# Kernel optimization log

Measured on AMD Instinct MI355X. Metric: run time of the kernel, lower is better.

Reference implementation:

```python
import jax, jax.numpy as jnp
import numpy as np

FEATURE_DIM = 16
NUM_HEADS = 16
HEAD_DIM = 64
R2 = float(np.sqrt(2.0))
RD = float(np.sqrt(FEATURE_DIM))        # sqrt(d) = 4
RRD = float(np.sqrt(RD))                # d^(1/4) = 2
RMS_EPS = 1e-5


def taylor_exp(x):
    # x: [b, h, l, d] -> [b, h, l, 1 + d + d*d]
    x2 = (x[..., :, None] * x[..., None, :]).reshape(*x.shape[:-1], FEATURE_DIM * FEATURE_DIM) / R2
    ones = jnp.ones_like(x[..., :1])
    return jnp.concatenate([ones, x / RRD, x2 / RD], axis=-1)


def setup_inputs() -> dict:
    key = jax.random.key(0)
    ks = jax.random.split(key, 5)
    b, l, d_model = 4, 2048, 1024
    inp = {
        'hidden_states': jax.random.normal(ks[0], (b, l, d_model), dtype=jnp.float32),
        'Wq': jax.random.normal(ks[1], (FEATURE_DIM * NUM_HEADS, d_model), dtype=jnp.float32) * 0.02,
        'Wk': jax.random.normal(ks[2], (FEATURE_DIM * NUM_HEADS, d_model), dtype=jnp.float32) * 0.02,
        'Wv': jax.random.normal(ks[3], (NUM_HEADS * HEAD_DIM, d_model), dtype=jnp.float32) * 0.02,
        'Wo': jax.random.normal(ks[4], (d_model, NUM_HEADS * HEAD_DIM), dtype=jnp.float32) * 0.02,
        'g_weight': jnp.ones((HEAD_DIM,), dtype=jnp.float32),
    }
    return inp


def reference(hidden_states, Wq, Wk, Wv, Wo, g_weight):
    b, l, _ = hidden_states.shape
    # projections (Linear, no bias): x @ W.T
    q = (hidden_states @ Wq.T).reshape(b, l, NUM_HEADS, FEATURE_DIM).transpose(0, 2, 1, 3)
    k = (hidden_states @ Wk.T).reshape(b, l, NUM_HEADS, FEATURE_DIM).transpose(0, 2, 1, 3)
    v = (hidden_states @ Wv.T).reshape(b, l, NUM_HEADS, HEAD_DIM).transpose(0, 2, 1, 3)

    qf = taylor_exp(q)  # [b, h, l, 273]
    kf = taylor_exp(k)  # [b, h, l, 273]

    A_qk = jnp.einsum('bhnd,bhmd->bhnm', qf, kf)
    A_qk = jnp.tril(A_qk)
    y = jnp.einsum('bhnm,bhme->bhne', A_qk, v)  # [b, h, l, head_dim]

    kv_state = jnp.einsum('bhnd,bhnf->bhfd', kf, v)[:, :, None]  # [b, h, 1, head_dim, 273]

    # RMSNorm over head_dim
    rms = jax.lax.rsqrt(jnp.mean(y * y, axis=-1, keepdims=True) + RMS_EPS)
    y = y * rms * g_weight

    y = y.transpose(0, 2, 1, 3).reshape(b, l, NUM_HEADS * HEAD_DIM)
    out = y @ Wo.T
    return out, kv_state
```

## Files before the change

kernel.cpp:

```cpp
#include <hip/hip_runtime.h>


typedef unsigned short u16;
typedef unsigned int u32;
typedef __attribute__((ext_vector_type(4))) float f32x4;
typedef __attribute__((ext_vector_type(16))) float f32x16;
typedef __attribute__((ext_vector_type(8))) short s16x8;

struct MaskT { static constexpr bool value = true;  };
struct MaskF { static constexpr bool value = false; };

__device__ __forceinline__ float bf2f(u16 u) {
    union { unsigned int i; float f; } x; x.i = ((unsigned int)u) << 16; return x.f;
}
__device__ __forceinline__ u16 f2bf(float f) {
    union { float f; unsigned int u; } x; x.f = f;
    unsigned int r = x.u + 0x7FFFu + ((x.u >> 16) & 1u);
    return (u16)(r >> 16);
}

typedef const __attribute__((address_space(1))) u32* gas1_t;
typedef __attribute__((address_space(3))) u32* las3_t;
__device__ __forceinline__ void gld16(const u16* g, u16* l) {
    __builtin_amdgcn_global_load_lds((gas1_t)(const void*)g, (las3_t)(void*)l, 16, 0, 0);
}

__global__ void detect_kernel(const unsigned int* __restrict__ H, int* __restrict__ flag)
{
    const int lane = threadIdx.x;
    int cnt = 0;
#pragma unroll
    for (int i = 0; i < 16; ++i) {
        const unsigned int wrd = H[lane * 16 + i];
        const int e = (int)((wrd >> 7) & 0xFFu);
        if (e >= 85 && e <= 170) ++cnt;
    }
    cnt += __shfl_xor(cnt, 1);  cnt += __shfl_xor(cnt, 2);
    cnt += __shfl_xor(cnt, 4);  cnt += __shfl_xor(cnt, 8);
    cnt += __shfl_xor(cnt, 16); cnt += __shfl_xor(cnt, 32);
    if (lane == 0) *flag = (cnt < 700) ? 1 : 0;
}

__global__ __launch_bounds__(256)
void cvt_all_kernel(const void* __restrict__ H,  const void* __restrict__ Wq,
                    const void* __restrict__ Wk, const void* __restrict__ Wv,
                    const void* __restrict__ Wo, const void* __restrict__ gw,
                    u16* __restrict__ Hb,  u16* __restrict__ Wqb,
                    u16* __restrict__ Wkb, u16* __restrict__ Wvb,
                    u16* __restrict__ Wob, u16* __restrict__ gwb,
                    const int* __restrict__ flag)
{
    const int f32in = *flag;
    const int NQ = 11010112 / 4;
    for (int qi = blockIdx.x * 256 + threadIdx.x; qi < NQ; qi += gridDim.x * 256) {
        const int i = qi * 4;
        const void* src; u16* dst; int off;
        if      (i <  8388608) { src = H;  dst = Hb;  off = i; }
        else if (i <  8650752) { src = Wq; dst = Wqb; off = i - 8388608; }
        else if (i <  8912896) { src = Wk; dst = Wkb; off = i - 8650752; }
        else if (i <  9961472) { src = Wv; dst = Wvb; off = i - 8912896; }
        else if (i < 11010048) { src = Wo; dst = Wob; off = i - 9961472; }
        else                   { src = gw; dst = gwb; off = i - 11010048; }
        ushort4 o;
        if (f32in) {
            const float4 v = *((const float4*)src + (off >> 2));
            o.x = f2bf(v.x); o.y = f2bf(v.y); o.z = f2bf(v.z); o.w = f2bf(v.w);
        } else {
            o = *((const ushort4*)src + (off >> 2));
        }
        *(ushort4*)(dst + off) = o;
    }
}

template<int MODE>
__global__ __launch_bounds__(256)
void gemm_nt(const u16* __restrict__ A,
             const u16* __restrict__ Bq, const u16* __restrict__ Bk,
             const u16* __restrict__ Bv,
             u16* __restrict__ Oq, u16* __restrict__ Ok,
             u16* __restrict__ Ovt, float* __restrict__ Of)
{
    __shared__ __attribute__((aligned(16))) u16 As[8192];
    __shared__ __attribute__((aligned(16))) u16 Bs[8192];
    const int t = threadIdx.x;
    const int lane = t & 63, w = t >> 6;
    const int c = lane & 15, qd = lane >> 4;
    const int wm = (w >> 1) * 64, wn = (w & 1) * 64;
    const int nwgx = gridDim.x;
    const int pid = blockIdx.y * nwgx + blockIdx.x;
    const int lid = (pid & 7) * ((nwgx * 64) >> 3) + (pid >> 3);
    const int rm = (lid / nwgx) * 128;
    const int cb = (lid % nwgx) * 128;

    const u16* Bsrc; int wrow0;
    if (MODE == 0) {
        if (cb < 256)      { Bsrc = Bq; wrow0 = cb; }
        else if (cb < 512) { Bsrc = Bk; wrow0 = cb - 256; }
        else               { Bsrc = Bv; wrow0 = cb - 512; }
    } else { Bsrc = Bq; wrow0 = cb; }

    f32x4 acc[4][4];
#pragma unroll
    for (int i = 0; i < 4; ++i)
#pragma unroll
        for (int j = 0; j < 4; ++j) acc[i][j] = (f32x4){0.f, 0.f, 0.f, 0.f};

    const int r0 = w * 8 + (lane >> 3);
    const int s0 = (lane & 7) ^ (lane >> 3);
    const u16* Ag = A    + (size_t)(rm    + r0) * 1024 + s0 * 8;
    const u16* Bg = Bsrc + (size_t)(wrow0 + r0) * 1024 + s0 * 8;
    u16* AsW = As + w * 512;
    u16* BsW = Bs + w * 512;

    for (int kt = 0; kt < 16; ++kt) {
        const int k0 = kt * 64;
        __syncthreads();
#pragma unroll
        for (int i = 0; i < 4; ++i) {
            gld16(Ag + (size_t)(i * 32) * 1024 + k0, AsW + i * 2048);
            gld16(Bg + (size_t)(i * 32) * 1024 + k0, BsW + i * 2048);
        }
        __syncthreads();
        s16x8 af[2][4], bfr[2][4];
#pragma unroll
        for (int kk = 0; kk < 2; ++kk) {
#pragma unroll
            for (int mt = 0; mt < 4; ++mt) {
                const int row = wm + mt * 16 + c;
                af[kk][mt] = *(const s16x8*)&As[row * 64 + (((kk * 4 + qd) ^ (row & 7)) * 8)];
            }
#pragma unroll
            for (int nt = 0; nt < 4; ++nt) {
                const int row = wn + nt * 16 + c;
                bfr[kk][nt] = *(const s16x8*)&Bs[row * 64 + (((kk * 4 + qd) ^ (row & 7)) * 8)];
            }
        }
#pragma unroll
        for (int kk = 0; kk < 2; ++kk)
#pragma unroll
            for (int mt = 0; mt < 4; ++mt)
#pragma unroll
                for (int nt = 0; nt < 4; ++nt)
                    acc[mt][nt] = __builtin_amdgcn_mfma_f32_16x16x32_bf16(af[kk][mt], bfr[kk][nt], acc[mt][nt], 0, 0, 0);
    }

#pragma unroll
    for (int mt = 0; mt < 4; ++mt) {
#pragma unroll
        for (int nt = 0; nt < 4; ++nt) {
            const int gc = cb + wn + nt * 16 + c;
            const int row0 = rm + wm + mt * 16 + qd * 4;
            if (MODE == 1) {
#pragma unroll
                for (int r = 0; r < 4; ++r)
                    Of[(size_t)(row0 + r) * 1024 + gc] = acc[mt][nt][r];
            } else if (gc < 512) {
#pragma unroll
                for (int r = 0; r < 4; ++r) {
                    const int row = row0 + r;
                    const int b_ = row >> 11, l_ = row & 2047;
                    const int cc = gc & 255;
                    const int h = cc >> 4, idx = cc & 15;
                    u16* dst = (gc < 256) ? Oq : Ok;
                    dst[(size_t)((b_ * 16 + h) * 2048 + l_) * 16 + idx] = f2bf(acc[mt][nt][r]);
                }
            } else {
                const int cc = gc - 512;
                const int h = cc >> 6, idx = cc & 63;
                const int b_ = row0 >> 11, l0 = row0 & 2047;
                ushort4 pk;
                pk.x = f2bf(acc[mt][nt][0]);
                pk.y = f2bf(acc[mt][nt][1]);
                pk.z = f2bf(acc[mt][nt][2]);
                pk.w = f2bf(acc[mt][nt][3]);
                *(ushort4*)(Ovt + ((size_t)((b_ * 16 + h) * 64 + idx)) * 2048 + l0) = pk;
            }
        }
    }
}

__global__ __launch_bounds__(512, 4)
void attn_kernel(const u16* __restrict__ Qg, const u16* __restrict__ Kg,
                 const u16* __restrict__ Vt, const u16* __restrict__ gwb,
                 u16* __restrict__ Yn)
{
    __shared__ __attribute__((aligned(16))) u16 Vs[2][8192];
    const int t = threadIdx.x, lane = t & 63, w = t >> 6;
    const int la = lane & 31, h = lane >> 5;
    const int pid = blockIdx.y * 8 + blockIdx.x;
    const int x = pid & 7;
    const int yy = pid >> 3;
    const int bh = x * 8 + (yy >> 3);
    const int jj = yy & 3;
    const int pass = (yy >> 2) & 1;
    const int qb = pass ? jj : (7 - jj);
    const int b_ = bh >> 4, hh = bh & 15;
    const u16* Qh = Qg + (size_t)bh * (2048 * 16);
    const u16* Kh = Kg + (size_t)bh * (2048 * 16);
    const u16* Vh = Vt + (size_t)bh * (64 * 2048);
    const float gl0 = bf2f(gwb[la]);
    const float gl1 = bf2f(gwb[32 + la]);
    const f32x16 z16 = {0.f,0.f,0.f,0.f,0.f,0.f,0.f,0.f,
                        0.f,0.f,0.f,0.f,0.f,0.f,0.f,0.f};
    const int vbase0 = (la << 8) | (h << 4);
    const int vsw = (la & 7) << 4;

    auto stageV = [&](int n0s, int bufsel) {
#pragma unroll
        for (int i = 0; i < 2; ++i) {
            const int slot = i * 512 + t;
            const int fl = slot >> 4;
            const int seg = (slot & 15) ^ (fl & 7);
            gld16(Vh + (size_t)fl * 2048 + n0s + seg * 8,
                  (u16*)Vs[bufsel] + (size_t)(i * 512 + (w << 6)) * 8);
        }
    };

    const int q0 = qb * 256 + w * 32;
    const int kf = 2 * qb + (w >> 2);
    const int wp = w & 3;
    const int nck = 2 * qb + 2;

    const s16x8 bq = *(const s16x8*)(Qh + (size_t)(q0 + la) * 16 + h * 8);
    f32x16 yt0 = z16, yt1 = z16;
    s16x8 ka[4];
    const char* vsc = (const char*)Vs[0];

    auto loadK = [&](s16x8* kk, int kcL) {
#pragma unroll
        for (int kt = 0; kt < 4; ++kt)
            kk[kt] = *(const s16x8*)(Kh + (size_t)(kcL * 128 + kt * 32 + la) * 16 + h * 8);
    };

    auto tile = [&](int kt, auto MASKED) {
        constexpr bool masked = decltype(MASKED)::value;
        f32x16 sv = __builtin_amdgcn_mfma_f32_32x32x16_bf16(ka[kt], bq, z16, 0, 0, 0);
        float p[16];
#pragma unroll
        for (int r = 0; r < 16; ++r) {
            const float s = sv[r];
            float pv = fmaf(s, fmaf(s, 0.03125f, 0.25f), 1.0f);
            if (masked) {
                const int keyloc = (r & 3) + 8 * (r >> 2) + 4 * h;
                if (keyloc > la) pv = 0.f;
            }
            p[r] = pv;
        }
#pragma unroll
        for (int ks = 0; ks < 2; ++ks) {
            u32 X0, X1, Y0, Y1;
            asm("v_cvt_pk_bf16_f32 %0, %1, %2" : "=v"(X0) : "v"(p[8*ks+0]), "v"(p[8*ks+1]));
            asm("v_cvt_pk_bf16_f32 %0, %1, %2" : "=v"(X1) : "v"(p[8*ks+2]), "v"(p[8*ks+3]));
            asm("v_cvt_pk_bf16_f32 %0, %1, %2" : "=v"(Y0) : "v"(p[8*ks+4]), "v"(p[8*ks+5]));
            asm("v_cvt_pk_bf16_f32 %0, %1, %2" : "=v"(Y1) : "v"(p[8*ks+6]), "v"(p[8*ks+7]));
            asm("v_permlane32_swap_b32 %0, %1" : "+v"(X0), "+v"(Y0));
            asm("v_permlane32_swap_b32 %0, %1" : "+v"(X1), "+v"(Y1));
            union { uint4 u; s16x8 v; } afu;
            afu.u = (uint4){X0, X1, Y0, Y1};
            const int offb = (kt << 6) | (ks << 5);
            const s16x8 vb0 = *(const s16x8*)(vsc + (((vbase0 + offb)) ^ vsw));
            const s16x8 vb1 = *(const s16x8*)(vsc + (((vbase0 + 8192 + offb)) ^ vsw));
            yt0 = __builtin_amdgcn_mfma_f32_32x32x16_bf16(afu.v, vb0, yt0, 0, 0, 0);
            yt1 = __builtin_amdgcn_mfma_f32_32x32x16_bf16(afu.v, vb1, yt1, 0, 0, 0);
        }
    };

    stageV(0, 0);
    loadK(ka, 0);
    __syncthreads();

    for (int kc = 0; kc < nck; ++kc) {
        const int cur = kc & 1;
        vsc = (const char*)Vs[cur];
        if (kc + 1 < nck) stageV((kc + 1) * 128, cur ^ 1);
        s16x8 kn[4] = {ka[0], ka[1], ka[2], ka[3]};
        if (kc < kf) loadK(kn, kc + 1);

        if (kc < kf) {
            tile(0, MaskF{}); tile(1, MaskF{});
            tile(2, MaskF{}); tile(3, MaskF{});
        } else if (kc == kf) {
            if (wp == 0)      { tile(0, MaskT{}); }
            else if (wp == 1) { tile(0, MaskF{}); tile(1, MaskT{}); }
            else if (wp == 2) { tile(0, MaskF{}); tile(1, MaskF{}); tile(2, MaskT{}); }
            else              { tile(0, MaskF{}); tile(1, MaskF{}); tile(2, MaskF{}); tile(3, MaskT{}); }
        }
        __syncthreads();
#pragma unroll
        for (int kt = 0; kt < 4; ++kt) ka[kt] = kn[kt];
    }

#pragma unroll
    for (int r = 0; r < 16; ++r) {
        float ss = yt0[r] * yt0[r] + yt1[r] * yt1[r];
        ss += __shfl_xor(ss, 1);  ss += __shfl_xor(ss, 2);
        ss += __shfl_xor(ss, 4);  ss += __shfl_xor(ss, 8);
        ss += __shfl_xor(ss, 16);
        const float rmsv = rsqrtf(ss * (1.0f / 64.0f) + 1e-5f);
        const int row = q0 + (r & 3) + 8 * (r >> 2) + 4 * h;
        u16* dst = Yn + ((size_t)(b_ * 2048 + row)) * 1024 + hh * 64;
        dst[la]      = f2bf(yt0[r] * rmsv * gl0);
        dst[32 + la] = f2bf(yt1[r] * rmsv * gl1);
    }
}

__global__ __launch_bounds__(256)
void kv_mfma_kernel(const u16* __restrict__ Kg, const u16* __restrict__ Vt,
                    float* __restrict__ kvpart)
{
    __shared__ __attribute__((aligned(16))) float kS[64][20];
    __shared__ __attribute__((aligned(16))) float kT[64][20];
    __shared__ __attribute__((aligned(16))) u16 KFs[288][72];
    __shared__ __attribute__((aligned(16))) u16 Vs[64][72];
    const int t = threadIdx.x, lane = t & 63, w = t >> 6;
    const int c = lane & 15, qd = lane >> 4;
    const int ns = blockIdx.x, bh = blockIdx.y;
    const u16* Kh  = Kg + (size_t)bh * 2048 * 16;
    const u16* Vth = Vt + (size_t)bh * 64 * 2048;

    int i2a, j2a, i2b = 18, j2b = 18;
    {
        const int dd = t;
        if (dd == 0)      { i2a = 16; j2a = 17; }
        else if (dd < 17) { i2a = dd - 1; j2a = 16; }
        else              { i2a = (dd - 17) >> 4; j2a = (dd - 17) & 15; }
        if (t < 32) {
            const int d2 = 256 + t;
            if (d2 < 273) { i2b = (d2 - 17) >> 4; j2b = (d2 - 17) & 15; }
        }
    }

    f32x4 acc[4][5];
#pragma unroll
    for (int mt = 0; mt < 4; ++mt)
#pragma unroll
        for (int j = 0; j < 5; ++j) acc[mt][j] = (f32x4){0.f, 0.f, 0.f, 0.f};

    for (int ch = 0; ch < 8; ++ch) {
        const int n0 = ns * 512 + ch * 64;
        __syncthreads();
        if (t < 128) {
            const int row = t >> 1, half = t & 1;
            uint4 kv = *(const uint4*)(Kh + (size_t)(n0 + row) * 16 + half * 8);
            const u16* ke = (const u16*)&kv;
#pragma unroll
            for (int e = 0; e < 8; ++e) {
                const float f = bf2f(ke[e]);
                kS[row][half * 8 + e] = f;
                kT[row][half * 8 + e] = f * 0.17677669529663687f;
            }
        } else if (t < 192) {
            const int row = t - 128;
            kS[row][16] = 1.f;  kS[row][17] = 1.f;  kS[row][18] = 0.f;
            kT[row][16] = 0.5f; kT[row][17] = 1.f;  kT[row][18] = 0.f;
        }
#pragma unroll
        for (int i = 0; i < 2; ++i) {
            const int lin = i * 256 + t;
            const int f = lin >> 3, seg = lin & 7;
            *(uint4*)&Vs[f][seg * 8] =
                *(const uint4*)(Vth + (size_t)f * 2048 + n0 + seg * 8);
        }
        __syncthreads();
        {
            unsigned int* dst = (unsigned int*)&KFs[t][0];
#pragma unroll 8
            for (int i = 0; i < 32; ++i) {
                const float v0 = kS[2 * i][i2a]     * kT[2 * i][j2a];
                const float v1 = kS[2 * i + 1][i2a] * kT[2 * i + 1][j2a];
                dst[i] = (unsigned int)f2bf(v0) | ((unsigned int)f2bf(v1) << 16);
            }
            if (t < 32) {
                unsigned int* dst2 = (unsigned int*)&KFs[256 + t][0];
#pragma unroll 8
                for (int i = 0; i < 32; ++i) {
                    const float v0 = kS[2 * i][i2b]     * kT[2 * i][j2b];
                    const float v1 = kS[2 * i + 1][i2b] * kT[2 * i + 1][j2b];
                    dst2[i] = (unsigned int)f2bf(v0) | ((unsigned int)f2bf(v1) << 16);
                }
            }
        }
        __syncthreads();
#pragma unroll
        for (int kt = 0; kt < 2; ++kt) {
            s16x8 va[4];
#pragma unroll
            for (int mt = 0; mt < 4; ++mt)
                va[mt] = *(const s16x8*)&Vs[mt * 16 + c][kt * 32 + qd * 8];
#pragma unroll
            for (int j = 0; j < 5; ++j) {
                const int dt = w + 4 * j;
                if (dt < 18) {
                    s16x8 vb = *(const s16x8*)&KFs[dt * 16 + c][kt * 32 + qd * 8];
#pragma unroll
                    for (int mt = 0; mt < 4; ++mt)
                        acc[mt][j] = __builtin_amdgcn_mfma_f32_16x16x32_bf16(va[mt], vb, acc[mt][j], 0, 0, 0);
                }
            }
        }
    }

    float* base = kvpart + ((size_t)(ns * 64 + bh) * 64) * 273;
#pragma unroll
    for (int j = 0; j < 5; ++j) {
        const int dt = w + 4 * j;
        if (dt >= 18) continue;
        const int dd = dt * 16 + c;
        if (dd >= 273) continue;
#pragma unroll
        for (int mt = 0; mt < 4; ++mt)
#pragma unroll
            for (int r = 0; r < 4; ++r) {
                const int f = mt * 16 + qd * 4 + r;
                base[f * 273 + dd] = acc[mt][j][r];
            }
    }
}

__global__ __launch_bounds__(256)
void kv_fin_kernel(const float* __restrict__ kvpart, float* __restrict__ o)
{
    const int i = blockIdx.x * 256 + threadIdx.x;
    const int S = 64 * 64 * 273;
    if (i < S)
        o[i] = kvpart[i] + kvpart[i + S] + kvpart[i + 2 * S] + kvpart[i + 3 * S];
}

extern "C" void kernel_launch(void* const* d_in, const int* in_sizes, int n_in,
                              void* d_out, int out_size, void* d_ws, size_t ws_size,
                              hipStream_t stream)
{
    const void* H  = d_in[0];
    const void* Wq = d_in[1];
    const void* Wk = d_in[2];
    const void* Wv = d_in[3];
    const void* Wo = d_in[4];
    const void* gw = d_in[5];
    float* outf = (float*)d_out;

    char* ws = (char*)d_ws;
    const size_t M = 1 << 20;
    u16*   Hb    = (u16*)(ws);
    u16*   Wqb   = (u16*)(ws + 16 * M);
    u16*   Wkb   = (u16*)(ws + 16 * M + 512 * 1024);
    u16*   Wvb   = (u16*)(ws + 17 * M);
    u16*   Wob   = (u16*)(ws + 19 * M);
    u16*   gwb   = (u16*)(ws + 21 * M);
    int*   flag  = (int*)(ws + 21 * M + 4096);
    u16*   q     = (u16*)(ws + 22 * M);
    u16*   k     = (u16*)(ws + 26 * M);
    u16*   vt    = (u16*)(ws + 30 * M);
    float* kvpart= (float*)(ws + 46 * M);
    u16*   yn    = Hb;

    detect_kernel<<<1, 64, 0, stream>>>((const unsigned int*)H, flag);
    cvt_all_kernel<<<2048, 256, 0, stream>>>(H, Wq, Wk, Wv, Wo, gw,
                                             Hb, Wqb, Wkb, Wvb, Wob, gwb, flag);

    gemm_nt<0><<<dim3(12, 64), 256, 0, stream>>>(Hb, Wqb, Wkb, Wvb, q, k, vt, nullptr);
    attn_kernel<<<dim3(8, 64), 512, 0, stream>>>(q, k, vt, gwb, yn);
    kv_mfma_kernel<<<dim3(4, 64), 256, 0, stream>>>(k, vt, kvpart);
    kv_fin_kernel<<<4368, 256, 0, stream>>>(kvpart, outf + (size_t)8388608);
    gemm_nt<1><<<dim3(8, 64), 256, 0, stream>>>(yn, Wob, nullptr, nullptr,
                                                nullptr, nullptr, nullptr, outf);
}
```

Before: 241.1 us.

## Fuse dtype detect and kv reduction into neighbors, merge attention passes per block

Folds the input-dtype detection into every block of the conversion kernel and the kv partial-sum reduction into the tail of the output-projection GEMM, removing two kernel launches. The attention kernel now runs both causal query-block passes (a long and a short one) inside a single workgroup, which halves the grid and balances work per block. It also relaxes launch bounds from 4 to 2 waves per SIMD and widens the LDS swizzle from 8 to 16 segments. The cost is less parallelism in attention and extra tail work in every GEMM block.

Measured after the change: 228.1 us. 5.4% less time.

```diff
diff --git a/kernel.cpp b/kernel.cpp
--- a/kernel.cpp
+++ b/kernel.cpp
@@ -23,22 +23,6 @@
 typedef __attribute__((address_space(3))) u32* las3_t;
 __device__ __forceinline__ void gld16(const u16* g, u16* l) {
     __builtin_amdgcn_global_load_lds((gas1_t)(const void*)g, (las3_t)(void*)l, 16, 0, 0);
-}
-
-__global__ void detect_kernel(const unsigned int* __restrict__ H, int* __restrict__ flag)
-{
-    const int lane = threadIdx.x;
-    int cnt = 0;
-#pragma unroll
-    for (int i = 0; i < 16; ++i) {
-        const unsigned int wrd = H[lane * 16 + i];
-        const int e = (int)((wrd >> 7) & 0xFFu);
-        if (e >= 85 && e <= 170) ++cnt;
-    }
-    cnt += __shfl_xor(cnt, 1);  cnt += __shfl_xor(cnt, 2);
-    cnt += __shfl_xor(cnt, 4);  cnt += __shfl_xor(cnt, 8);
-    cnt += __shfl_xor(cnt, 16); cnt += __shfl_xor(cnt, 32);
-    if (lane == 0) *flag = (cnt < 700) ? 1 : 0;
 }
 
 __global__ __launch_bounds__(256)
@@ -47,12 +31,29 @@
                     const void* __restrict__ Wo, const void* __restrict__ gw,
                     u16* __restrict__ Hb,  u16* __restrict__ Wqb,
                     u16* __restrict__ Wkb, u16* __restrict__ Wvb,
-                    u16* __restrict__ Wob, u16* __restrict__ gwb,
-                    const int* __restrict__ flag)
+                    u16* __restrict__ Wob, u16* __restrict__ gwb)
 {
-    const int f32in = *flag;
+    __shared__ int sflag;
+    const int t = threadIdx.x;
+    if (t < 64) {
+        const unsigned int* Hw = (const unsigned int*)H;
+        int cnt = 0;
+#pragma unroll
+        for (int i = 0; i < 16; ++i) {
+            const unsigned int wrd = Hw[t * 16 + i];
+            const int e = (int)((wrd >> 7) & 0xFFu);
+            if (e >= 85 && e <= 170) ++cnt;
+        }
+        cnt += __shfl_xor(cnt, 1);  cnt += __shfl_xor(cnt, 2);
+        cnt += __shfl_xor(cnt, 4);  cnt += __shfl_xor(cnt, 8);
+        cnt += __shfl_xor(cnt, 16); cnt += __shfl_xor(cnt, 32);
+        if (t == 0) sflag = (cnt < 700) ? 1 : 0;
+    }
+    __syncthreads();
+    const int f32in = sflag;
+
     const int NQ = 11010112 / 4;
-    for (int qi = blockIdx.x * 256 + threadIdx.x; qi < NQ; qi += gridDim.x * 256) {
+    for (int qi = blockIdx.x * 256 + t; qi < NQ; qi += gridDim.x * 256) {
         const int i = qi * 4;
         const void* src; u16* dst; int off;
         if      (i <  8388608) { src = H;  dst = Hb;  off = i; }
@@ -78,7 +79,8 @@
              const u16* __restrict__ Bq, const u16* __restrict__ Bk,
              const u16* __restrict__ Bv,
              u16* __restrict__ Oq, u16* __restrict__ Ok,
-             u16* __restrict__ Ovt, float* __restrict__ Of)
+             u16* __restrict__ Ovt, float* __restrict__ Of,
+             const float* __restrict__ Kvp, float* __restrict__ Kvo)
 {
     __shared__ __attribute__((aligned(16))) u16 As[8192];
     __shared__ __attribute__((aligned(16))) u16 Bs[8192];
@@ -177,9 +179,24 @@
             }
         }
     }
-}
-
-__global__ __launch_bounds__(512, 4)
+
+    if (MODE == 1) {
+        const int S = 64 * 64 * 273;
+        const int NQ4 = S / 4;
+        const int NT = gridDim.x * gridDim.y * 256;
+        for (int q = pid * 256 + t; q < NQ4; q += NT) {
+            float4 a = ((const float4*)Kvp)[q];
+            const float4 b = ((const float4*)(Kvp + S))[q];
+            const float4 c2 = ((const float4*)(Kvp + 2 * S))[q];
+            const float4 d = ((const float4*)(Kvp + 3 * S))[q];
+            a.x += b.x + c2.x + d.x;  a.y += b.y + c2.y + d.y;
+            a.z += b.z + c2.z + d.z;  a.w += b.w + c2.w + d.w;
+            ((float4*)Kvo)[q] = a;
+        }
+    }
+}
+
+__global__ __launch_bounds__(512, 2)
 void attn_kernel(const u16* __restrict__ Qg, const u16* __restrict__ Kg,
                  const u16* __restrict__ Vt, const u16* __restrict__ gwb,
                  u16* __restrict__ Yn)
@@ -187,13 +204,10 @@
     __shared__ __attribute__((aligned(16))) u16 Vs[2][8192];
     const int t = threadIdx.x, lane = t & 63, w = t >> 6;
     const int la = lane & 31, h = lane >> 5;
-    const int pid = blockIdx.y * 8 + blockIdx.x;
-    const int x = pid & 7;
-    const int yy = pid >> 3;
-    const int bh = x * 8 + (yy >> 3);
-    const int jj = yy & 3;
-    const int pass = (yy >> 2) & 1;
-    const int qb = pass ? jj : (7 - jj);
+    const int pid = blockIdx.y * 4 + blockIdx.x;
+    const int lid = (pid & 7) * 32 + (pid >> 3);
+    const int bh = lid >> 2;
+    const int jj = lid & 3;
     const int b_ = bh >> 4, hh = bh & 15;
     const u16* Qh = Qg + (size_t)bh * (2048 * 16);
     const u16* Kh = Kg + (size_t)bh * (2048 * 16);
@@ -203,104 +217,107 @@
     const f32x16 z16 = {0.f,0.f,0.f,0.f,0.f,0.f,0.f,0.f,
                         0.f,0.f,0.f,0.f,0.f,0.f,0.f,0.f};
     const int vbase0 = (la << 8) | (h << 4);
-    const int vsw = (la & 7) << 4;
+    const int vsw = (la & 15) << 4;
 
     auto stageV = [&](int n0s, int bufsel) {
 #pragma unroll
         for (int i = 0; i < 2; ++i) {
             const int slot = i * 512 + t;
             const int fl = slot >> 4;
-            const int seg = (slot & 15) ^ (fl & 7);
+            const int seg = (slot & 15) ^ (fl & 15);
             gld16(Vh + (size_t)fl * 2048 + n0s + seg * 8,
                   (u16*)Vs[bufsel] + (size_t)(i * 512 + (w << 6)) * 8);
         }
     };
 
-    const int q0 = qb * 256 + w * 32;
-    const int kf = 2 * qb + (w >> 2);
-    const int wp = w & 3;
-    const int nck = 2 * qb + 2;
-
-    const s16x8 bq = *(const s16x8*)(Qh + (size_t)(q0 + la) * 16 + h * 8);
-    f32x16 yt0 = z16, yt1 = z16;
-    s16x8 ka[4];
-    const char* vsc = (const char*)Vs[0];
-
-    auto loadK = [&](s16x8* kk, int kcL) {
-#pragma unroll
-        for (int kt = 0; kt < 4; ++kt)
-            kk[kt] = *(const s16x8*)(Kh + (size_t)(kcL * 128 + kt * 32 + la) * 16 + h * 8);
-    };
-
-    auto tile = [&](int kt, auto MASKED) {
-        constexpr bool masked = decltype(MASKED)::value;
-        f32x16 sv = __builtin_amdgcn_mfma_f32_32x32x16_bf16(ka[kt], bq, z16, 0, 0, 0);
-        float p[16];
+    for (int pass = 0; pass < 2; ++pass) {
+        const int qb = pass ? jj : (7 - jj);
+        const int q0 = qb * 256 + w * 32;
+        const int kf = 2 * qb + (w >> 2);
+        const int wp = w & 3;
+        const int nck = 2 * qb + 2;
+
+        const s16x8 bq = *(const s16x8*)(Qh + (size_t)(q0 + la) * 16 + h * 8);
+        f32x16 yt0 = z16, yt1 = z16;
+        s16x8 ka[4];
+        const char* vsc = (const char*)Vs[0];
+
+        auto loadK = [&](s16x8* kk, int kcL) {
+#pragma unroll
+            for (int kt = 0; kt < 4; ++kt)
+                kk[kt] = *(const s16x8*)(Kh + (size_t)(kcL * 128 + kt * 32 + la) * 16 + h * 8);
+        };
+
+        auto tile = [&](int kt, auto MASKED) {
+            constexpr bool masked = decltype(MASKED)::value;
+            f32x16 sv = __builtin_amdgcn_mfma_f32_32x32x16_bf16(ka[kt], bq, z16, 0, 0, 0);
+            float p[16];
+#pragma unroll
+            for (int r = 0; r < 16; ++r) {
+                const float s = sv[r];
+                float pv = fmaf(s, fmaf(s, 0.03125f, 0.25f), 1.0f);
+                if (masked) {
+                    const int keyloc = (r & 3) + 8 * (r >> 2) + 4 * h;
+                    if (keyloc > la) pv = 0.f;
+                }
+                p[r] = pv;
+            }
+#pragma unroll
+            for (int ks = 0; ks < 2; ++ks) {
+                u32 X0, X1, Y0, Y1;
+                asm("v_cvt_pk_bf16_f32 %0, %1, %2" : "=v"(X0) : "v"(p[8*ks+0]), "v"(p[8*ks+1]));
+                asm("v_cvt_pk_bf16_f32 %0, %1, %2" : "=v"(X1) : "v"(p[8*ks+2]), "v"(p[8*ks+3]));
+                asm("v_cvt_pk_bf16_f32 %0, %1, %2" : "=v"(Y0) : "v"(p[8*ks+4]), "v"(p[8*ks+5]));
+                asm("v_cvt_pk_bf16_f32 %0, %1, %2" : "=v"(Y1) : "v"(p[8*ks+6]), "v"(p[8*ks+7]));
+                asm("v_permlane32_swap_b32 %0, %1" : "+v"(X0), "+v"(Y0));
+                asm("v_permlane32_swap_b32 %0, %1" : "+v"(X1), "+v"(Y1));
+                union { uint4 u; s16x8 v; } afu;
+                afu.u = (uint4){X0, X1, Y0, Y1};
+                const int offb = (kt << 6) | (ks << 5);
+                const s16x8 vb0 = *(const s16x8*)(vsc + (((vbase0 + offb)) ^ vsw));
+                const s16x8 vb1 = *(const s16x8*)(vsc + (((vbase0 + 8192 + offb)) ^ vsw));
+                yt0 = __builtin_amdgcn_mfma_f32_32x32x16_bf16(afu.v, vb0, yt0, 0, 0, 0);
+                yt1 = __builtin_amdgcn_mfma_f32_32x32x16_bf16(afu.v, vb1, yt1, 0, 0, 0);
+            }
+        };
+
+        stageV(0, 0);
+        loadK(ka, 0);
+        __syncthreads();
+
+        for (int kc = 0; kc < nck; ++kc) {
+            const int cur = kc & 1;
+            vsc = (const char*)Vs[cur];
+            if (kc + 1 < nck) stageV((kc + 1) * 128, cur ^ 1);
+            s16x8 kn[4] = {ka[0], ka[1], ka[2], ka[3]};
+            if (kc < kf) loadK(kn, kc + 1);
+
+            if (kc < kf) {
+                tile(0, MaskF{}); tile(1, MaskF{});
+                tile(2, MaskF{}); tile(3, MaskF{});
+            } else if (kc == kf) {
+                if (wp == 0)      { tile(0, MaskT{}); }
+                else if (wp == 1) { tile(0, MaskF{}); tile(1, MaskT{}); }
+                else if (wp == 2) { tile(0, MaskF{}); tile(1, MaskF{}); tile(2, MaskT{}); }
+                else              { tile(0, MaskF{}); tile(1, MaskF{}); tile(2, MaskF{}); tile(3, MaskT{}); }
+            }
+            __syncthreads();
+#pragma unroll
+            for (int kt = 0; kt < 4; ++kt) ka[kt] = kn[kt];
+        }
+
 #pragma unroll
         for (int r = 0; r < 16; ++r) {
-            const float s = sv[r];
-            float pv = fmaf(s, fmaf(s, 0.03125f, 0.25f), 1.0f);
-            if (masked) {
-                const int keyloc = (r & 3) + 8 * (r >> 2) + 4 * h;
-                if (keyloc > la) pv = 0.f;
-            }
-            p[r] = pv;
-        }
-#pragma unroll
-        for (int ks = 0; ks < 2; ++ks) {
-            u32 X0, X1, Y0, Y1;
-            asm("v_cvt_pk_bf16_f32 %0, %1, %2" : "=v"(X0) : "v"(p[8*ks+0]), "v"(p[8*ks+1]));
-            asm("v_cvt_pk_bf16_f32 %0, %1, %2" : "=v"(X1) : "v"(p[8*ks+2]), "v"(p[8*ks+3]));
-            asm("v_cvt_pk_bf16_f32 %0, %1, %2" : "=v"(Y0) : "v"(p[8*ks+4]), "v"(p[8*ks+5]));
-            asm("v_cvt_pk_bf16_f32 %0, %1, %2" : "=v"(Y1) : "v"(p[8*ks+6]), "v"(p[8*ks+7]));
-            asm("v_permlane32_swap_b32 %0, %1" : "+v"(X0), "+v"(Y0));
-            asm("v_permlane32_swap_b32 %0, %1" : "+v"(X1), "+v"(Y1));
-            union { uint4 u; s16x8 v; } afu;
-            afu.u = (uint4){X0, X1, Y0, Y1};
-            const int offb = (kt << 6) | (ks << 5);
-            const s16x8 vb0 = *(const s16x8*)(vsc + (((vbase0 + offb)) ^ vsw));
-            const s16x8 vb1 = *(const s16x8*)(vsc + (((vbase0 + 8192 + offb)) ^ vsw));
-            yt0 = __builtin_amdgcn_mfma_f32_32x32x16_bf16(afu.v, vb0, yt0, 0, 0, 0);
-            yt1 = __builtin_amdgcn_mfma_f32_32x32x16_bf16(afu.v, vb1, yt1, 0, 0, 0);
-        }
-    };
-
-    stageV(0, 0);
-    loadK(ka, 0);
-    __syncthreads();
-
-    for (int kc = 0; kc < nck; ++kc) {
-        const int cur = kc & 1;
-        vsc = (const char*)Vs[cur];
-        if (kc + 1 < nck) stageV((kc + 1) * 128, cur ^ 1);
-        s16x8 kn[4] = {ka[0], ka[1], ka[2], ka[3]};
-        if (kc < kf) loadK(kn, kc + 1);
-
-        if (kc < kf) {
-            tile(0, MaskF{}); tile(1, MaskF{});
-            tile(2, MaskF{}); tile(3, MaskF{});
-        } else if (kc == kf) {
-            if (wp == 0)      { tile(0, MaskT{}); }
-            else if (wp == 1) { tile(0, MaskF{}); tile(1, MaskT{}); }
-            else if (wp == 2) { tile(0, MaskF{}); tile(1, MaskF{}); tile(2, MaskT{}); }
-            else              { tile(0, MaskF{}); tile(1, MaskF{}); tile(2, MaskF{}); tile(3, MaskT{}); }
-        }
-        __syncthreads();
-#pragma unroll
-        for (int kt = 0; kt < 4; ++kt) ka[kt] = kn[kt];
-    }
-
-#pragma unroll
-    for (int r = 0; r < 16; ++r) {
-        float ss = yt0[r] * yt0[r] + yt1[r] * yt1[r];
-        ss += __shfl_xor(ss, 1);  ss += __shfl_xor(ss, 2);
-        ss += __shfl_xor(ss, 4);  ss += __shfl_xor(ss, 8);
-        ss += __shfl_xor(ss, 16);
-        const float rmsv = rsqrtf(ss * (1.0f / 64.0f) + 1e-5f);
-        const int row = q0 + (r & 3) + 8 * (r >> 2) + 4 * h;
-        u16* dst = Yn + ((size_t)(b_ * 2048 + row)) * 1024 + hh * 64;
-        dst[la]      = f2bf(yt0[r] * rmsv * gl0);
-        dst[32 + la] = f2bf(yt1[r] * rmsv * gl1);
+            float ss = yt0[r] * yt0[r] + yt1[r] * yt1[r];
+            ss += __shfl_xor(ss, 1);  ss += __shfl_xor(ss, 2);
+            ss += __shfl_xor(ss, 4);  ss += __shfl_xor(ss, 8);
+            ss += __shfl_xor(ss, 16);
+            const float rmsv = rsqrtf(ss * (1.0f / 64.0f) + 1e-5f);
+            const int row = q0 + (r & 3) + 8 * (r >> 2) + 4 * h;
+            u16* dst = Yn + ((size_t)(b_ * 2048 + row)) * 1024 + hh * 64;
+            dst[la]      = f2bf(yt0[r] * rmsv * gl0);
+            dst[32 + la] = f2bf(yt1[r] * rmsv * gl1);
+        }
     }
 }
 
@@ -417,15 +434,6 @@
     }
 }
 
-__global__ __launch_bounds__(256)
-void kv_fin_kernel(const float* __restrict__ kvpart, float* __restrict__ o)
-{
-    const int i = blockIdx.x * 256 + threadIdx.x;
-    const int S = 64 * 64 * 273;
-    if (i < S)
-        o[i] = kvpart[i] + kvpart[i + S] + kvpart[i + 2 * S] + kvpart[i + 3 * S];
-}
-
 extern "C" void kernel_launch(void* const* d_in, const int* in_sizes, int n_in,
                               void* d_out, int out_size, void* d_ws, size_t ws_size,
                               hipStream_t stream)
@@ -446,21 +454,20 @@
     u16*   Wvb   = (u16*)(ws + 17 * M);
     u16*   Wob   = (u16*)(ws + 19 * M);
     u16*   gwb   = (u16*)(ws + 21 * M);
-    int*   flag  = (int*)(ws + 21 * M + 4096);
     u16*   q     = (u16*)(ws + 22 * M);
     u16*   k     = (u16*)(ws + 26 * M);
     u16*   vt    = (u16*)(ws + 30 * M);
     float* kvpart= (float*)(ws + 46 * M);
     u16*   yn    = Hb;
 
-    detect_kernel<<<1, 64, 0, stream>>>((const unsigned int*)H, flag);
     cvt_all_kernel<<<2048, 256, 0, stream>>>(H, Wq, Wk, Wv, Wo, gw,
-                                             Hb, Wqb, Wkb, Wvb, Wob, gwb, flag);
-
-    gemm_nt<0><<<dim3(12, 64), 256, 0, stream>>>(Hb, Wqb, Wkb, Wvb, q, k, vt, nullptr);
-    attn_kernel<<<dim3(8, 64), 512, 0, stream>>>(q, k, vt, gwb, yn);
+                                             Hb, Wqb, Wkb, Wvb, Wob, gwb);
+
+    gemm_nt<0><<<dim3(12, 64), 256, 0, stream>>>(Hb, Wqb, Wkb, Wvb, q, k, vt,
+                                                 nullptr, nullptr, nullptr);
+    attn_kernel<<<dim3(4, 64), 512, 0, stream>>>(q, k, vt, gwb, yn);
     kv_mfma_kernel<<<dim3(4, 64), 256, 0, stream>>>(k, vt, kvpart);
-    kv_fin_kernel<<<4368, 256, 0, stream>>>(kvpart, outf + (size_t)8388608);
     gemm_nt<1><<<dim3(8, 64), 256, 0, stream>>>(yn, Wob, nullptr, nullptr,
-                                                nullptr, nullptr, nullptr, outf);
-}
+                                                nullptr, nullptr, nullptr, outf,
+                                                kvpart, outf + (size_t)8388608);
+}
```
